# Kernel optimization log

Measured on AMD Instinct MI355X. Metric: run time of the kernel, lower is better.

Reference implementation:

```python
import jax, jax.numpy as jnp
import numpy as np

N = 100000       # nodes
E = 1600000      # edges (avg degree 16)
F_IN, HID, C, K = 64, 64, 16, 3


def setup_inputs() -> dict:
    key = jax.random.key(0)
    ks = jax.random.split(key, 4)
    x = jax.random.normal(ks[0], (N, F_IN), dtype=jnp.float32)
    edge_index = jax.random.randint(ks[1], (2, E), 0, N, dtype=jnp.int32)
    s1 = 1.0 / np.sqrt(F_IN)
    W1 = jax.random.uniform(ks[2], (K, F_IN, HID), jnp.float32, -s1, s1)
    b1 = jnp.zeros((HID,), jnp.float32)
    s2 = 1.0 / np.sqrt(HID)
    W2 = jax.random.uniform(ks[3], (K, HID, C), jnp.float32, -s2, s2)
    b2 = jnp.zeros((C,), jnp.float32)
    return {"x": x, "edge_index": edge_index, "W1": W1, "b1": b1, "W2": W2, "b2": b2}


def _cheb_conv(x, row, col, wedge, W, b):
    """PyG ChebConv with sym norm, lambda_max=2: L_hat = -D^-1/2 A D^-1/2."""
    prop = lambda h: jax.ops.segment_sum(h[col] * wedge[:, None], row, num_segments=N)
    Tx0 = x
    out = Tx0 @ W[0]
    Tx1 = prop(x)
    out = out + Tx1 @ W[1]
    for k in range(2, W.shape[0]):
        Tx2 = 2.0 * prop(Tx1) - Tx0
        out = out + Tx2 @ W[k]
        Tx0, Tx1 = Tx1, Tx2
    return out + b


def reference(x, edge_index, W1, b1, W2, b2):
    row, col = edge_index[0], edge_index[1]
    deg = jax.ops.segment_sum(jnp.ones((edge_index.shape[1],), x.dtype), row, num_segments=N)
    dinv = jnp.where(deg > 0, jax.lax.rsqrt(jnp.maximum(deg, 1.0)), 0.0)
    wedge = -dinv[row] * dinv[col]  # scaled-Laplacian edge weights
    h = jax.nn.relu(_cheb_conv(x, row, col, wedge, W1, b1))
    # dropout: identity in eval mode
    out = _cheb_conv(h, row, col, wedge, W2, b2)
    return jax.nn.log_softmax(out, axis=1)
```

## Files before the change

kernel.cpp:

```cpp
#include <hip/hip_runtime.h>

#define NN 100000
#define NE 1600000
#define NBUCK 391
#define CAP 5632

typedef __attribute__((ext_vector_type(8))) short bf16x8;
typedef __attribute__((ext_vector_type(4))) short bf16x4;
typedef __attribute__((ext_vector_type(4))) float f32x4;

__device__ inline unsigned short f2bf(float f) {
    unsigned int u = __float_as_uint(f);
    return (unsigned short)((u + 0x7FFFu + ((u >> 16) & 1u)) >> 16);
}
__device__ inline float bf2f(short s) {
    return __uint_as_float(((unsigned int)(unsigned short)s) << 16);
}

__global__ __launch_bounds__(256) void k_bin(const int* __restrict__ row, const int* __restrict__ col,
                                             int* __restrict__ gcursor, int* __restrict__ ebuf) {
    __shared__ int hist[NBUCK];
    for (int i = threadIdx.x; i < NBUCK; i += 256) hist[i] = 0;
    __syncthreads();
    int start = blockIdx.x * 3125;
    int end = start + 3125; if (end > NE) end = NE;
    for (int e = start + threadIdx.x; e < end; e += 256)
        atomicAdd(&hist[row[e] >> 8], 1);
    __syncthreads();
    for (int i = threadIdx.x; i < NBUCK; i += 256)
        hist[i] = atomicAdd(&gcursor[i], hist[i]);
    __syncthreads();
    for (int e = start + threadIdx.x; e < end; e += 256) {
        int r = row[e], c = col[e];
        int bk = r >> 8;
        int pos = atomicAdd(&hist[bk], 1);
        if (pos < CAP) ebuf[bk * CAP + pos] = (c << 8) | (r & 255);
    }
}

__global__ void k_bstart(const int* __restrict__ gcursor, int* __restrict__ bstart,
                         int* __restrict__ row_ptr) {
    __shared__ int s[512];
    int t = threadIdx.x;
    int d = (t < NBUCK) ? gcursor[t] : 0;
    s[t] = d; __syncthreads();
    for (int off = 1; off < 512; off <<= 1) {
        int v = (t >= off) ? s[t - off] : 0;
        __syncthreads();
        s[t] += v;
        __syncthreads();
    }
    if (t < NBUCK) bstart[t] = s[t] - d;
    if (t == NBUCK - 1) bstart[NBUCK] = s[t];
    if (t == 0) row_ptr[NN] = NE;
}

__global__ __launch_bounds__(256) void k_build(const int* __restrict__ ebuf, const int* __restrict__ bstart,
                                               int* __restrict__ row_ptr, float* __restrict__ dinv,
                                               int* __restrict__ col_sorted) {
    __shared__ int deg[256], cur[256], ps[256];
    int b = blockIdx.x;
    int bs = bstart[b], cnt = bstart[b + 1] - bs;
    const int* eb = ebuf + (size_t)b * CAP;
    int t = threadIdx.x;
    deg[t] = 0;
    __syncthreads();
    for (int e = t; e < cnt; e += 256)
        atomicAdd(&deg[eb[e] & 255], 1);
    __syncthreads();
    int d = deg[t];
    ps[t] = d; __syncthreads();
    for (int off = 1; off < 256; off <<= 1) {
        int v = (t >= off) ? ps[t - off] : 0;
        __syncthreads();
        ps[t] += v;
        __syncthreads();
    }
    int base = bs + ps[t] - d;
    cur[t] = base;
    int n = (b << 8) + t;
    if (n < NN) {
        row_ptr[n] = base;
        dinv[n] = d > 0 ? rsqrtf((float)d) : 0.f;
    }
    __syncthreads();
    for (int e = t; e < cnt; e += 256) {
        int w = eb[e];
        int pos = atomicAdd(&cur[w & 255], 1);
        col_sorted[pos] = ((unsigned)w) >> 8;
    }
}

__global__ void k_scale(const float* __restrict__ x, const float* __restrict__ dinv,
                        unsigned short* __restrict__ xsbf, unsigned short* __restrict__ xbf) {
    int t = blockIdx.x * 256 + threadIdx.x;
    if (t < NN * 16) {
        float d = dinv[t >> 4];
        float4 v = ((const float4*)x)[t];
        bf16x4 u, s;
        u[0] = (short)f2bf(v.x); u[1] = (short)f2bf(v.y); u[2] = (short)f2bf(v.z); u[3] = (short)f2bf(v.w);
        s[0] = (short)f2bf(v.x * d); s[1] = (short)f2bf(v.y * d); s[2] = (short)f2bf(v.z * d); s[3] = (short)f2bf(v.w * d);
        ((bf16x4*)xbf)[t] = u;
        ((bf16x4*)xsbf)[t] = s;
    }
}

__global__ __launch_bounds__(256) void k_spmm64b(const unsigned short* __restrict__ ins,
                                                 const unsigned short* __restrict__ subbf,
                                                 unsigned short* __restrict__ outb,
                                                 unsigned short* __restrict__ outsb,
                                                 const int* __restrict__ row_ptr, const int* __restrict__ cs,
                                                 const float* __restrict__ dinv,
                                                 int has_sub, int has_outs) {
    int n = blockIdx.x * 4 + (threadIdx.x >> 6);
    if (n >= NN) return;
    int nu = __builtin_amdgcn_readfirstlane(n);
    int lane = threadIdx.x & 63;
    int es = lane >> 3;
    int f = lane & 7;
    int s = row_ptr[nu], e = row_ptr[nu + 1];
    float a0[8] = {0,0,0,0,0,0,0,0}, a1[8] = {0,0,0,0,0,0,0,0};
    int i = s;
    for (; i + 15 < e; i += 16) {
        int c0 = cs[i + es];
        int c1 = cs[i + 8 + es];
        bf16x8 v0 = *((const bf16x8*)(ins + (size_t)c0 * 64 + f * 8));
        bf16x8 v1 = *((const bf16x8*)(ins + (size_t)c1 * 64 + f * 8));
        #pragma unroll
        for (int j = 0; j < 8; ++j) { a0[j] += bf2f(v0[j]); a1[j] += bf2f(v1[j]); }
    }
    for (; i + es < e; i += 8) {
        int c0 = cs[i + es];
        bf16x8 v0 = *((const bf16x8*)(ins + (size_t)c0 * 64 + f * 8));
        #pragma unroll
        for (int j = 0; j < 8; ++j) a0[j] += bf2f(v0[j]);
    }
    float a[8];
    #pragma unroll
    for (int j = 0; j < 8; ++j) {
        a[j] = a0[j] + a1[j];
        a[j] += __shfl_xor(a[j], 8);
        a[j] += __shfl_xor(a[j], 16);
        a[j] += __shfl_xor(a[j], 32);
    }
    if (es == 0) {
        float dn = dinv[nu];
        float r[8];
        #pragma unroll
        for (int j = 0; j < 8; ++j) r[j] = -dn * a[j];
        if (has_sub) {
            bf16x8 sv = *((const bf16x8*)(subbf + (size_t)nu * 64 + f * 8));
            #pragma unroll
            for (int j = 0; j < 8; ++j) r[j] = 2.f * r[j] - bf2f(sv[j]);
        }
        bf16x8 ob;
        #pragma unroll
        for (int j = 0; j < 8; ++j) ob[j] = (short)f2bf(r[j]);
        *((bf16x8*)(outb + (size_t)nu * 64 + f * 8)) = ob;
        if (has_outs) {
            bf16x8 os;
            #pragma unroll
            for (int j = 0; j < 8; ++j) os[j] = (short)f2bf(dn * r[j]);
            *((bf16x8*)(outsb + (size_t)nu * 64 + f * 8)) = os;
        }
    }
}

__global__ __launch_bounds__(256) void k_d1p(const unsigned short* __restrict__ xbf,
                                             const unsigned short* __restrict__ t1bf,
                                             const unsigned short* __restrict__ t2bf,
                                             const float* __restrict__ W1, const float* __restrict__ b1,
                                             const float* __restrict__ W2, const float* __restrict__ b2,
                                             const float* __restrict__ dinv,
                                             float* __restrict__ Apre, unsigned short* __restrict__ Gsb) {
    __shared__ unsigned short Wf1[24 * 64 * 8];
    __shared__ unsigned short Wf2[6 * 64 * 8];
    __shared__ unsigned short Ht[4][1024];
    for (int slot = threadIdx.x; slot < 24 * 64; slot += 256) {
        int c = slot / 384;
        int t = (slot / 64) % 6;
        int l = slot & 63;
        int rr = l & 15, gg = l >> 4;
        unsigned int pk[4];
        #pragma unroll
        for (int jp = 0; jp < 4; ++jp) {
            int k0 = t * 32 + gg * 8 + jp * 2;
            unsigned int lo = f2bf(W1[(k0 >> 6) * 4096 + (k0 & 63) * 64 + c * 16 + rr]);
            int k1 = k0 + 1;
            unsigned int hi = f2bf(W1[(k1 >> 6) * 4096 + (k1 & 63) * 64 + c * 16 + rr]);
            pk[jp] = lo | (hi << 16);
        }
        *((uint4*)&Wf1[slot * 8]) = *((uint4*)pk);
    }
    for (int slot = threadIdx.x; slot < 6 * 64; slot += 256) {
        int c = slot / 128;
        int t = (slot / 64) & 1;
        int l = slot & 63;
        int rr = l & 15, gg = l >> 4;
        unsigned int pk[4];
        #pragma unroll
        for (int jp = 0; jp < 4; ++jp) {
            int k0 = t * 32 + gg * 8 + jp * 2;
            int k1 = k0 + 1;
            float w0, w1;
            if (c == 0)      { w0 = W2[k0 * 16 + rr] - W2[2048 + k0 * 16 + rr];
                               w1 = W2[k1 * 16 + rr] - W2[2048 + k1 * 16 + rr]; }
            else if (c == 1) { w0 = W2[1024 + k0 * 16 + rr]; w1 = W2[1024 + k1 * 16 + rr]; }
            else             { w0 = W2[2048 + k0 * 16 + rr]; w1 = W2[2048 + k1 * 16 + rr]; }
            pk[jp] = (unsigned int)f2bf(w0) | ((unsigned int)f2bf(w1) << 16);
        }
        *((uint4*)&Wf2[slot * 8]) = *((uint4*)pk);
    }
    __syncthreads();

    int lane = threadIdx.x & 63;
    int r = lane & 15, g = lane >> 4;
    int widx = threadIdx.x >> 6;
    char* ht = (char*)Ht[widx];

    bf16x8 bfr1[4][6];
    #pragma unroll
    for (int c = 0; c < 4; ++c)
        #pragma unroll
        for (int t = 0; t < 6; ++t)
            bfr1[c][t] = *((const bf16x8*)&Wf1[((c * 6 + t) * 64 + lane) * 8]);
    bf16x8 bfr2[3][2];
    #pragma unroll
    for (int c = 0; c < 3; ++c)
        #pragma unroll
        for (int t = 0; t < 2; ++t)
            bfr2[c][t] = *((const bf16x8*)&Wf2[((c * 2 + t) * 64 + lane) * 8]);

    float bl[4];
    #pragma unroll
    for (int c = 0; c < 4; ++c) bl[c] = b1[c * 16 + r];
    float b2r = b2[r];

    const unsigned short* arrs[3] = {xbf, t1bf, t2bf};
    int wid = blockIdx.x * 4 + widx;
    int wstride = gridDim.x * 4;
    for (int tile = wid; tile < NN / 16; tile += wstride) {
        int nb = tile * 16;
        bf16x8 af[6];
        #pragma unroll
        for (int t = 0; t < 6; ++t)
            af[t] = *((const bf16x8*)(arrs[t >> 1] + (size_t)(nb + r) * 64 + (t & 1) * 32 + g * 8));
        f32x4 acc[4];
        #pragma unroll
        for (int c = 0; c < 4; ++c) acc[c] = (f32x4){bl[c], bl[c], bl[c], bl[c]};
        #pragma unroll
        for (int t = 0; t < 6; ++t)
            #pragma unroll
            for (int c = 0; c < 4; ++c)
                acc[c] = __builtin_amdgcn_mfma_f32_16x16x32_bf16(af[t], bfr1[c][t], acc[c], 0, 0, 0);
        #pragma unroll
        for (int c = 0; c < 4; ++c)
            #pragma unroll
            for (int q = 0; q < 4; ++q) {
                int node = g * 4 + q;
                int byte = (node * 64 + c * 16 + r) * 2;
                byte ^= (node & 7) << 4;
                *((unsigned short*)(ht + byte)) = f2bf(fmaxf(acc[c][q], 0.f));
            }
        bf16x8 af2[2];
        #pragma unroll
        for (int t = 0; t < 2; ++t) {
            int byte = (r * 64 + t * 32 + g * 8) * 2;
            byte ^= (r & 7) << 4;
            af2[t] = *((const bf16x8*)(ht + byte));
        }
        f32x4 acc2[3];
        #pragma unroll
        for (int c = 0; c < 3; ++c) acc2[c] = (f32x4){0.f, 0.f, 0.f, 0.f};
        #pragma unroll
        for (int t = 0; t < 2; ++t)
            #pragma unroll
            for (int c = 0; c < 3; ++c)
                acc2[c] = __builtin_amdgcn_mfma_f32_16x16x32_bf16(af2[t], bfr2[c][t], acc2[c], 0, 0, 0);
        #pragma unroll
        for (int q = 0; q < 4; ++q) {
            int n = nb + g * 4 + q;
            float dv = dinv[n];
            Apre[(size_t)n * 16 + r] = acc2[0][q] + b2r;
            Gsb[(size_t)n * 32 + r]      = f2bf(acc2[1][q] * dv);
            Gsb[(size_t)n * 32 + 16 + r] = f2bf(acc2[2][q] * dv);
        }
    }
}

__global__ __launch_bounds__(256) void k_spmm32b(const unsigned short* __restrict__ Gsb,
                                                 float* __restrict__ q1, unsigned short* __restrict__ tsb,
                                                 const int* __restrict__ row_ptr, const int* __restrict__ cs,
                                                 const float* __restrict__ dinv) {
    int n = blockIdx.x * 4 + (threadIdx.x >> 6);
    if (n >= NN) return;
    int nu = __builtin_amdgcn_readfirstlane(n);
    int lane = threadIdx.x & 63;
    int es = lane >> 3;
    int f = lane & 7;
    int s = row_ptr[nu], e = row_ptr[nu + 1];
    float a0[4] = {0,0,0,0}, a1[4] = {0,0,0,0};
    int i = s;
    for (; i + 15 < e; i += 16) {
        int c0 = cs[i + es];
        int c1 = cs[i + 8 + es];
        bf16x4 v0 = *((const bf16x4*)(Gsb + (size_t)c0 * 32 + f * 4));
        bf16x4 v1 = *((const bf16x4*)(Gsb + (size_t)c1 * 32 + f * 4));
        #pragma unroll
        for (int j = 0; j < 4; ++j) { a0[j] += bf2f(v0[j]); a1[j] += bf2f(v1[j]); }
    }
    for (; i + es < e; i += 8) {
        int c0 = cs[i + es];
        bf16x4 v0 = *((const bf16x4*)(Gsb + (size_t)c0 * 32 + f * 4));
        #pragma unroll
        for (int j = 0; j < 4; ++j) a0[j] += bf2f(v0[j]);
    }
    float a[4];
    #pragma unroll
    for (int j = 0; j < 4; ++j) {
        a[j] = a0[j] + a1[j];
        a[j] += __shfl_xor(a[j], 8);
        a[j] += __shfl_xor(a[j], 16);
        a[j] += __shfl_xor(a[j], 32);
    }
    if (es == 0) {
        float dn = dinv[nu];
        if (f < 4) {
            float4 w;
            w.x = -dn * a[0]; w.y = -dn * a[1]; w.z = -dn * a[2]; w.w = -dn * a[3];
            *((float4*)(q1 + (size_t)nu * 16 + f * 4)) = w;
        } else {
            bf16x4 w;
            #pragma unroll
            for (int j = 0; j < 4; ++j) w[j] = (short)f2bf(dn * (-dn * a[j]));
            *((bf16x4*)(tsb + (size_t)nu * 16 + (f - 4) * 4)) = w;
        }
    }
}

__global__ __launch_bounds__(256) void k_spmm16f(const unsigned short* __restrict__ tsb,
                                                 const float* __restrict__ Apre, const float* __restrict__ q1,
                                                 const int* __restrict__ row_ptr, const int* __restrict__ cs,
                                                 const float* __restrict__ dinv, float* __restrict__ out) {
    int n = blockIdx.x * 4 + (threadIdx.x >> 6);
    if (n >= NN) return;
    int nu = __builtin_amdgcn_readfirstlane(n);
    int lane = threadIdx.x & 63;
    int es = lane >> 2;
    int f = lane & 3;
    int s = row_ptr[nu], e = row_ptr[nu + 1];
    float a0[4] = {0,0,0,0}, a1[4] = {0,0,0,0};
    int i = s;
    for (; i + 31 < e; i += 32) {
        int c0 = cs[i + es];
        int c1 = cs[i + 16 + es];
        bf16x4 v0 = *((const bf16x4*)(tsb + (size_t)c0 * 16 + f * 4));
        bf16x4 v1 = *((const bf16x4*)(tsb + (size_t)c1 * 16 + f * 4));
        #pragma unroll
        for (int j = 0; j < 4; ++j) { a0[j] += bf2f(v0[j]); a1[j] += bf2f(v1[j]); }
    }
    for (; i + es < e; i += 16) {
        int c0 = cs[i + es];
        bf16x4 v0 = *((const bf16x4*)(tsb + (size_t)c0 * 16 + f * 4));
        #pragma unroll
        for (int j = 0; j < 4; ++j) a0[j] += bf2f(v0[j]);
    }
    float a[4];
    #pragma unroll
    for (int j = 0; j < 4; ++j) {
        a[j] = a0[j] + a1[j];
        a[j] += __shfl_xor(a[j], 4);
        a[j] += __shfl_xor(a[j], 8);
        a[j] += __shfl_xor(a[j], 16);
        a[j] += __shfl_xor(a[j], 32);
    }
    if (es == 0) {
        float dn = dinv[nu];
        float o[4];
        #pragma unroll
        for (int j = 0; j < 4; ++j)
            o[j] = Apre[(size_t)nu * 16 + f * 4 + j] + q1[(size_t)nu * 16 + f * 4 + j]
                   + 2.f * (-dn * a[j]);
        float m = fmaxf(fmaxf(o[0], o[1]), fmaxf(o[2], o[3]));
        m = fmaxf(m, __shfl_xor(m, 1));
        m = fmaxf(m, __shfl_xor(m, 2));
        float ssum = expf(o[0] - m) + expf(o[1] - m) + expf(o[2] - m) + expf(o[3] - m);
        ssum += __shfl_xor(ssum, 1);
        ssum += __shfl_xor(ssum, 2);
        float ls = logf(ssum);
        float4 w;
        w.x = o[0] - m - ls; w.y = o[1] - m - ls; w.z = o[2] - m - ls; w.w = o[3] - m - ls;
        *((float4*)(out + (size_t)nu * 16 + f * 4)) = w;
    }
}

extern "C" void kernel_launch(void* const* d_in, const int* in_sizes, int n_in,
                              void* d_out, int out_size, void* d_ws, size_t ws_size,
                              hipStream_t stream) {
    const float* x  = (const float*)d_in[0];
    const int*   ei = (const int*)d_in[1];
    const int*   row = ei;
    const int*   col = ei + NE;
    const float* W1 = (const float*)d_in[2];
    const float* b1 = (const float*)d_in[3];
    const float* W2 = (const float*)d_in[4];
    const float* b2 = (const float*)d_in[5];
    float* out = (float*)d_out;

    char* base = (char*)d_ws;
    size_t off = 0;
    auto alloc = [&](size_t bytes) -> char* {
        char* r = base + off;
        off = (off + bytes + 255) & ~(size_t)255;
        return r;
    };
    int*   gcursor    = (int*)alloc(NBUCK * 4);
    int*   bstart     = (int*)alloc((NBUCK + 1) * 4);
    float* dinv       = (float*)alloc((size_t)NN * 4);
    int*   row_ptr    = (int*)alloc((size_t)(NN + 1) * 4);
    int*   ebuf       = (int*)alloc((size_t)NBUCK * CAP * 4);
    int*   col_sorted = (int*)alloc((size_t)NE * 4);
    unsigned short* Xbf  = (unsigned short*)alloc((size_t)NN * 64 * 2);
    unsigned short* XSbf = (unsigned short*)alloc((size_t)NN * 64 * 2);
    unsigned short* T1bf = (unsigned short*)alloc((size_t)NN * 64 * 2);
    unsigned short* T1s  = (unsigned short*)alloc((size_t)NN * 64 * 2);
    unsigned short* T2bf = (unsigned short*)alloc((size_t)NN * 64 * 2);
    float* Apre          = (float*)alloc((size_t)NN * 16 * 4);
    unsigned short* Gsb  = (unsigned short*)alloc((size_t)NN * 32 * 2);
    float* q1            = (float*)alloc((size_t)NN * 16 * 4);
    unsigned short* tsb  = (unsigned short*)alloc((size_t)NN * 16 * 2);

    hipMemsetAsync(gcursor, 0, NBUCK * 4, stream);

    k_bin<<<512, 256, 0, stream>>>(row, col, gcursor, ebuf);
    k_bstart<<<1, 512, 0, stream>>>(gcursor, bstart, row_ptr);
    k_build<<<NBUCK, 256, 0, stream>>>(ebuf, bstart, row_ptr, dinv, col_sorted);
    k_scale<<<(NN * 16 + 255) / 256, 256, 0, stream>>>(x, dinv, XSbf, Xbf);

    int nbS = (NN + 3) / 4;
    k_spmm64b<<<nbS, 256, 0, stream>>>(XSbf, nullptr, T1bf, T1s, row_ptr, col_sorted, dinv, 0, 1);
    k_spmm64b<<<nbS, 256, 0, stream>>>(T1s, Xbf, T2bf, nullptr, row_ptr, col_sorted, dinv, 1, 0);
    k_d1p<<<625, 256, 0, stream>>>(Xbf, T1bf, T2bf, W1, b1, W2, b2, dinv, Apre, Gsb);
    k_spmm32b<<<nbS, 256, 0, stream>>>(Gsb, q1, tsb, row_ptr, col_sorted, dinv);
    k_spmm16f<<<nbS, 256, 0, stream>>>(tsb, Apre, q1, row_ptr, col_sorted, dinv, out);
}
```

Before: 235.6 us.

## Drop T1 buffer via sqrt-degree rescale, bf16 intermediates, nontemporal hints

The first SpMM no longer writes the unscaled T1 array. The dense layer reads the dinv-scaled T1s instead and multiplies that partial GEMM result by sqrt(deg) per node, using a separate accumulator. Apre and q1 intermediates are now stored as bf16 instead of fp32, and nontemporal load/store hints are added across the streaming accesses. These changes cut global memory traffic, at the cost of some extra rounding error from bf16 storage and from rescaling after bf16 quantisation.

```diff
diff --git a/kernel.cpp b/kernel.cpp
--- a/kernel.cpp
+++ b/kernel.cpp
@@ -57,7 +57,7 @@
 
 __global__ __launch_bounds__(256) void k_build(const int* __restrict__ ebuf, const int* __restrict__ bstart,
                                                int* __restrict__ row_ptr, float* __restrict__ dinv,
-                                               int* __restrict__ col_sorted) {
+                                               float* __restrict__ rdeg, int* __restrict__ col_sorted) {
     __shared__ int deg[256], cur[256], ps[256];
     int b = blockIdx.x;
     int bs = bstart[b], cnt = bstart[b + 1] - bs;
@@ -82,12 +82,13 @@
     if (n < NN) {
         row_ptr[n] = base;
         dinv[n] = d > 0 ? rsqrtf((float)d) : 0.f;
+        rdeg[n] = sqrtf((float)d);
     }
     __syncthreads();
     for (int e = t; e < cnt; e += 256) {
         int w = eb[e];
         int pos = atomicAdd(&cur[w & 255], 1);
-        col_sorted[pos] = ((unsigned)w) >> 8;
+        __builtin_nontemporal_store(((unsigned)w) >> 8, &col_sorted[pos]);
     }
 }
 
@@ -96,12 +97,12 @@
     int t = blockIdx.x * 256 + threadIdx.x;
     if (t < NN * 16) {
         float d = dinv[t >> 4];
-        float4 v = ((const float4*)x)[t];
+        f32x4 v = __builtin_nontemporal_load(&((const f32x4*)x)[t]);
         bf16x4 u, s;
-        u[0] = (short)f2bf(v.x); u[1] = (short)f2bf(v.y); u[2] = (short)f2bf(v.z); u[3] = (short)f2bf(v.w);
-        s[0] = (short)f2bf(v.x * d); s[1] = (short)f2bf(v.y * d); s[2] = (short)f2bf(v.z * d); s[3] = (short)f2bf(v.w * d);
-        ((bf16x4*)xbf)[t] = u;
-        ((bf16x4*)xsbf)[t] = s;
+        u[0] = (short)f2bf(v[0]); u[1] = (short)f2bf(v[1]); u[2] = (short)f2bf(v[2]); u[3] = (short)f2bf(v[3]);
+        s[0] = (short)f2bf(v[0] * d); s[1] = (short)f2bf(v[1] * d); s[2] = (short)f2bf(v[2] * d); s[3] = (short)f2bf(v[3] * d);
+        __builtin_nontemporal_store(u, &((bf16x4*)xbf)[t]);
+        __builtin_nontemporal_store(s, &((bf16x4*)xsbf)[t]);
     }
 }
 
@@ -111,7 +112,7 @@
                                                  unsigned short* __restrict__ outsb,
                                                  const int* __restrict__ row_ptr, const int* __restrict__ cs,
                                                  const float* __restrict__ dinv,
-                                                 int has_sub, int has_outs) {
+                                                 int has_sub, int has_outb, int has_outs) {
     int n = blockIdx.x * 4 + (threadIdx.x >> 6);
     if (n >= NN) return;
     int nu = __builtin_amdgcn_readfirstlane(n);
@@ -122,15 +123,15 @@
     float a0[8] = {0,0,0,0,0,0,0,0}, a1[8] = {0,0,0,0,0,0,0,0};
     int i = s;
     for (; i + 15 < e; i += 16) {
-        int c0 = cs[i + es];
-        int c1 = cs[i + 8 + es];
+        int c0 = __builtin_nontemporal_load(&cs[i + es]);
+        int c1 = __builtin_nontemporal_load(&cs[i + 8 + es]);
         bf16x8 v0 = *((const bf16x8*)(ins + (size_t)c0 * 64 + f * 8));
         bf16x8 v1 = *((const bf16x8*)(ins + (size_t)c1 * 64 + f * 8));
         #pragma unroll
         for (int j = 0; j < 8; ++j) { a0[j] += bf2f(v0[j]); a1[j] += bf2f(v1[j]); }
     }
     for (; i + es < e; i += 8) {
-        int c0 = cs[i + es];
+        int c0 = __builtin_nontemporal_load(&cs[i + es]);
         bf16x8 v0 = *((const bf16x8*)(ins + (size_t)c0 * 64 + f * 8));
         #pragma unroll
         for (int j = 0; j < 8; ++j) a0[j] += bf2f(v0[j]);
@@ -149,30 +150,32 @@
         #pragma unroll
         for (int j = 0; j < 8; ++j) r[j] = -dn * a[j];
         if (has_sub) {
-            bf16x8 sv = *((const bf16x8*)(subbf + (size_t)nu * 64 + f * 8));
+            bf16x8 sv = __builtin_nontemporal_load((const bf16x8*)(subbf + (size_t)nu * 64 + f * 8));
             #pragma unroll
             for (int j = 0; j < 8; ++j) r[j] = 2.f * r[j] - bf2f(sv[j]);
         }
-        bf16x8 ob;
-        #pragma unroll
-        for (int j = 0; j < 8; ++j) ob[j] = (short)f2bf(r[j]);
-        *((bf16x8*)(outb + (size_t)nu * 64 + f * 8)) = ob;
+        if (has_outb) {
+            bf16x8 ob;
+            #pragma unroll
+            for (int j = 0; j < 8; ++j) ob[j] = (short)f2bf(r[j]);
+            __builtin_nontemporal_store(ob, (bf16x8*)(outb + (size_t)nu * 64 + f * 8));
+        }
         if (has_outs) {
             bf16x8 os;
             #pragma unroll
             for (int j = 0; j < 8; ++j) os[j] = (short)f2bf(dn * r[j]);
-            *((bf16x8*)(outsb + (size_t)nu * 64 + f * 8)) = os;
+            __builtin_nontemporal_store(os, (bf16x8*)(outsb + (size_t)nu * 64 + f * 8));
         }
     }
 }
 
 __global__ __launch_bounds__(256) void k_d1p(const unsigned short* __restrict__ xbf,
-                                             const unsigned short* __restrict__ t1bf,
+                                             const unsigned short* __restrict__ t1s,
                                              const unsigned short* __restrict__ t2bf,
                                              const float* __restrict__ W1, const float* __restrict__ b1,
                                              const float* __restrict__ W2, const float* __restrict__ b2,
-                                             const float* __restrict__ dinv,
-                                             float* __restrict__ Apre, unsigned short* __restrict__ Gsb) {
+                                             const float* __restrict__ dinv, const float* __restrict__ rdeg,
+                                             unsigned short* __restrict__ Apreb, unsigned short* __restrict__ Gsb) {
     __shared__ unsigned short Wf1[24 * 64 * 8];
     __shared__ unsigned short Wf2[6 * 64 * 8];
     __shared__ unsigned short Ht[4][1024];
@@ -236,7 +239,7 @@
     for (int c = 0; c < 4; ++c) bl[c] = b1[c * 16 + r];
     float b2r = b2[r];
 
-    const unsigned short* arrs[3] = {xbf, t1bf, t2bf};
+    const unsigned short* arrs[3] = {xbf, t1s, t2bf};
     int wid = blockIdx.x * 4 + widx;
     int wstride = gridDim.x * 4;
     for (int tile = wid; tile < NN / 16; tile += wstride) {
@@ -245,22 +248,33 @@
         #pragma unroll
         for (int t = 0; t < 6; ++t)
             af[t] = *((const bf16x8*)(arrs[t >> 1] + (size_t)(nb + r) * 64 + (t & 1) * 32 + g * 8));
-        f32x4 acc[4];
-        #pragma unroll
-        for (int c = 0; c < 4; ++c) acc[c] = (f32x4){bl[c], bl[c], bl[c], bl[c]};
-        #pragma unroll
-        for (int t = 0; t < 6; ++t)
-            #pragma unroll
-            for (int c = 0; c < 4; ++c)
-                acc[c] = __builtin_amdgcn_mfma_f32_16x16x32_bf16(af[t], bfr1[c][t], acc[c], 0, 0, 0);
+        f32x4 acc[4], accT[4];
+        #pragma unroll
+        for (int c = 0; c < 4; ++c) {
+            acc[c] = (f32x4){bl[c], bl[c], bl[c], bl[c]};
+            accT[c] = (f32x4){0.f, 0.f, 0.f, 0.f};
+        }
+        #pragma unroll
+        for (int c = 0; c < 4; ++c) {
+            acc[c]  = __builtin_amdgcn_mfma_f32_16x16x32_bf16(af[0], bfr1[c][0], acc[c], 0, 0, 0);
+            acc[c]  = __builtin_amdgcn_mfma_f32_16x16x32_bf16(af[1], bfr1[c][1], acc[c], 0, 0, 0);
+            accT[c] = __builtin_amdgcn_mfma_f32_16x16x32_bf16(af[2], bfr1[c][2], accT[c], 0, 0, 0);
+            accT[c] = __builtin_amdgcn_mfma_f32_16x16x32_bf16(af[3], bfr1[c][3], accT[c], 0, 0, 0);
+            acc[c]  = __builtin_amdgcn_mfma_f32_16x16x32_bf16(af[4], bfr1[c][4], acc[c], 0, 0, 0);
+            acc[c]  = __builtin_amdgcn_mfma_f32_16x16x32_bf16(af[5], bfr1[c][5], acc[c], 0, 0, 0);
+        }
+        float rdq[4];
+        #pragma unroll
+        for (int q = 0; q < 4; ++q) rdq[q] = rdeg[nb + g * 4 + q];
         #pragma unroll
         for (int c = 0; c < 4; ++c)
             #pragma unroll
             for (int q = 0; q < 4; ++q) {
+                float hval = fmaxf(acc[c][q] + rdq[q] * accT[c][q], 0.f);
                 int node = g * 4 + q;
                 int byte = (node * 64 + c * 16 + r) * 2;
                 byte ^= (node & 7) << 4;
-                *((unsigned short*)(ht + byte)) = f2bf(fmaxf(acc[c][q], 0.f));
+                *((unsigned short*)(ht + byte)) = f2bf(hval);
             }
         bf16x8 af2[2];
         #pragma unroll
@@ -281,15 +295,15 @@
         for (int q = 0; q < 4; ++q) {
             int n = nb + g * 4 + q;
             float dv = dinv[n];
-            Apre[(size_t)n * 16 + r] = acc2[0][q] + b2r;
-            Gsb[(size_t)n * 32 + r]      = f2bf(acc2[1][q] * dv);
-            Gsb[(size_t)n * 32 + 16 + r] = f2bf(acc2[2][q] * dv);
+            __builtin_nontemporal_store(f2bf(acc2[0][q] + b2r), &Apreb[(size_t)n * 16 + r]);
+            __builtin_nontemporal_store(f2bf(acc2[1][q] * dv), &Gsb[(size_t)n * 32 + r]);
+            __builtin_nontemporal_store(f2bf(acc2[2][q] * dv), &Gsb[(size_t)n * 32 + 16 + r]);
         }
     }
 }
 
 __global__ __launch_bounds__(256) void k_spmm32b(const unsigned short* __restrict__ Gsb,
-                                                 float* __restrict__ q1, unsigned short* __restrict__ tsb,
+                                                 unsigned short* __restrict__ q1b, unsigned short* __restrict__ tsb,
                                                  const int* __restrict__ row_ptr, const int* __restrict__ cs,
                                                  const float* __restrict__ dinv) {
     int n = blockIdx.x * 4 + (threadIdx.x >> 6);
@@ -302,15 +316,15 @@
     float a0[4] = {0,0,0,0}, a1[4] = {0,0,0,0};
     int i = s;
     for (; i + 15 < e; i += 16) {
-        int c0 = cs[i + es];
-        int c1 = cs[i + 8 + es];
+        int c0 = __builtin_nontemporal_load(&cs[i + es]);
+        int c1 = __builtin_nontemporal_load(&cs[i + 8 + es]);
         bf16x4 v0 = *((const bf16x4*)(Gsb + (size_t)c0 * 32 + f * 4));
         bf16x4 v1 = *((const bf16x4*)(Gsb + (size_t)c1 * 32 + f * 4));
         #pragma unroll
         for (int j = 0; j < 4; ++j) { a0[j] += bf2f(v0[j]); a1[j] += bf2f(v1[j]); }
     }
     for (; i + es < e; i += 8) {
-        int c0 = cs[i + es];
+        int c0 = __builtin_nontemporal_load(&cs[i + es]);
         bf16x4 v0 = *((const bf16x4*)(Gsb + (size_t)c0 * 32 + f * 4));
         #pragma unroll
         for (int j = 0; j < 4; ++j) a0[j] += bf2f(v0[j]);
@@ -326,20 +340,22 @@
     if (es == 0) {
         float dn = dinv[nu];
         if (f < 4) {
-            float4 w;
-            w.x = -dn * a[0]; w.y = -dn * a[1]; w.z = -dn * a[2]; w.w = -dn * a[3];
-            *((float4*)(q1 + (size_t)nu * 16 + f * 4)) = w;
+            bf16x4 w;
+            #pragma unroll
+            for (int j = 0; j < 4; ++j) w[j] = (short)f2bf(-dn * a[j]);
+            __builtin_nontemporal_store(w, (bf16x4*)(q1b + (size_t)nu * 16 + f * 4));
         } else {
             bf16x4 w;
             #pragma unroll
             for (int j = 0; j < 4; ++j) w[j] = (short)f2bf(dn * (-dn * a[j]));
-            *((bf16x4*)(tsb + (size_t)nu * 16 + (f - 4) * 4)) = w;
+            __builtin_nontemporal_store(w, (bf16x4*)(tsb + (size_t)nu * 16 + (f - 4) * 4));
         }
     }
 }
 
 __global__ __launch_bounds__(256) void k_spmm16f(const unsigned short* __restrict__ tsb,
-                                                 const float* __restrict__ Apre, const float* __restrict__ q1,
+                                                 const unsigned short* __restrict__ Apreb,
+                                                 const unsigned short* __restrict__ q1b,
                                                  const int* __restrict__ row_ptr, const int* __restrict__ cs,
                                                  const float* __restrict__ dinv, float* __restrict__ out) {
     int n = blockIdx.x * 4 + (threadIdx.x >> 6);
@@ -352,15 +368,15 @@
     float a0[4] = {0,0,0,0}, a1[4] = {0,0,0,0};
     int i = s;
     for (; i + 31 < e; i += 32) {
-        int c0 = cs[i + es];
-        int c1 = cs[i + 16 + es];
+        int c0 = __builtin_nontemporal_load(&cs[i + es]);
+        int c1 = __builtin_nontemporal_load(&cs[i + 16 + es]);
         bf16x4 v0 = *((const bf16x4*)(tsb + (size_t)c0 * 16 + f * 4));
         bf16x4 v1 = *((const bf16x4*)(tsb + (size_t)c1 * 16 + f * 4));
         #pragma unroll
         for (int j = 0; j < 4; ++j) { a0[j] += bf2f(v0[j]); a1[j] += bf2f(v1[j]); }
     }
     for (; i + es < e; i += 16) {
-        int c0 = cs[i + es];
+        int c0 = __builtin_nontemporal_load(&cs[i + es]);
         bf16x4 v0 = *((const bf16x4*)(tsb + (size_t)c0 * 16 + f * 4));
         #pragma unroll
         for (int j = 0; j < 4; ++j) a0[j] += bf2f(v0[j]);
@@ -376,11 +392,12 @@
     }
     if (es == 0) {
         float dn = dinv[nu];
+        bf16x4 ap = *((const bf16x4*)(Apreb + (size_t)nu * 16 + f * 4));
+        bf16x4 qv = *((const bf16x4*)(q1b + (size_t)nu * 16 + f * 4));
         float o[4];
         #pragma unroll
         for (int j = 0; j < 4; ++j)
-            o[j] = Apre[(size_t)nu * 16 + f * 4 + j] + q1[(size_t)nu * 16 + f * 4 + j]
-                   + 2.f * (-dn * a[j]);
+            o[j] = bf2f(ap[j]) + bf2f(qv[j]) + 2.f * (-dn * a[j]);
         float m = fmaxf(fmaxf(o[0], o[1]), fmaxf(o[2], o[3]));
         m = fmaxf(m, __shfl_xor(m, 1));
         m = fmaxf(m, __shfl_xor(m, 2));
@@ -388,9 +405,9 @@
         ssum += __shfl_xor(ssum, 1);
         ssum += __shfl_xor(ssum, 2);
         float ls = logf(ssum);
-        float4 w;
-        w.x = o[0] - m - ls; w.y = o[1] - m - ls; w.z = o[2] - m - ls; w.w = o[3] - m - ls;
-        *((float4*)(out + (size_t)nu * 16 + f * 4)) = w;
+        f32x4 w;
+        w[0] = o[0] - m - ls; w[1] = o[1] - m - ls; w[2] = o[2] - m - ls; w[3] = o[3] - m - ls;
+        __builtin_nontemporal_store(w, (f32x4*)(out + (size_t)nu * 16 + f * 4));
     }
 }
 
@@ -417,30 +434,30 @@
     int*   gcursor    = (int*)alloc(NBUCK * 4);
     int*   bstart     = (int*)alloc((NBUCK + 1) * 4);
     float* dinv       = (float*)alloc((size_t)NN * 4);
+    float* rdeg       = (float*)alloc((size_t)NN * 4);
     int*   row_ptr    = (int*)alloc((size_t)(NN + 1) * 4);
     int*   ebuf       = (int*)alloc((size_t)NBUCK * CAP * 4);
     int*   col_sorted = (int*)alloc((size_t)NE * 4);
     unsigned short* Xbf  = (unsigned short*)alloc((size_t)NN * 64 * 2);
     unsigned short* XSbf = (unsigned short*)alloc((size_t)NN * 64 * 2);
-    unsigned short* T1bf = (unsigned short*)alloc((size_t)NN * 64 * 2);
     unsigned short* T1s  = (unsigned short*)alloc((size_t)NN * 64 * 2);
     unsigned short* T2bf = (unsigned short*)alloc((size_t)NN * 64 * 2);
-    float* Apre          = (float*)alloc((size_t)NN * 16 * 4);
+    unsigned short* Apreb = (unsigned short*)alloc((size_t)NN * 16 * 2);
     unsigned short* Gsb  = (unsigned short*)alloc((size_t)NN * 32 * 2);
-    float* q1            = (float*)alloc((size_t)NN * 16 * 4);
+    unsigned short* q1b  = (unsigned short*)alloc((size_t)NN * 16 * 2);
     unsigned short* tsb  = (unsigned short*)alloc((size_t)NN * 16 * 2);
 
     hipMemsetAsync(gcursor, 0, NBUCK * 4, stream);
 
     k_bin<<<512, 256, 0, stream>>>(row, col, gcursor, ebuf);
     k_bstart<<<1, 512, 0, stream>>>(gcursor, bstart, row_ptr);
-    k_build<<<NBUCK, 256, 0, stream>>>(ebuf, bstart, row_ptr, dinv, col_sorted);
+    k_build<<<NBUCK, 256, 0, stream>>>(ebuf, bstart, row_ptr, dinv, rdeg, col_sorted);
     k_scale<<<(NN * 16 + 255) / 256, 256, 0, stream>>>(x, dinv, XSbf, Xbf);
 
     int nbS = (NN + 3) / 4;
-    k_spmm64b<<<nbS, 256, 0, stream>>>(XSbf, nullptr, T1bf, T1s, row_ptr, col_sorted, dinv, 0, 1);
-    k_spmm64b<<<nbS, 256, 0, stream>>>(T1s, Xbf, T2bf, nullptr, row_ptr, col_sorted, dinv, 1, 0);
-    k_d1p<<<625, 256, 0, stream>>>(Xbf, T1bf, T2bf, W1, b1, W2, b2, dinv, Apre, Gsb);
-    k_spmm32b<<<nbS, 256, 0, stream>>>(Gsb, q1, tsb, row_ptr, col_sorted, dinv);
-    k_spmm16f<<<nbS, 256, 0, stream>>>(tsb, Apre, q1, row_ptr, col_sorted, dinv, out);
-}
+    k_spmm64b<<<nbS, 256, 0, stream>>>(XSbf, nullptr, nullptr, T1s, row_ptr, col_sorted, dinv, 0, 0, 1);
+    k_spmm64b<<<nbS, 256, 0, stream>>>(T1s, Xbf, T2bf, nullptr, row_ptr, col_sorted, dinv, 1, 1, 0);
+    k_d1p<<<625, 256, 0, stream>>>(Xbf, T1s, T2bf, W1, b1, W2, b2, dinv, rdeg, Apreb, Gsb);
+    k_spmm32b<<<nbS, 256, 0, stream>>>(Gsb, q1b, tsb, row_ptr, col_sorted, dinv);
+    k_spmm16f<<<nbS, 256, 0, stream>>>(tsb, Apreb, q1b, row_ptr, col_sorted, dinv, out);
+}
```

Result: slower. 282.2 us (+19.8%).
